# Kernel tuning notes

Hardware: AMD Instinct MI355X
Metric: run time of the kernel (lower is better)

Reference implementation:

```python
import jax, jax.numpy as jnp
import numpy as np
import math

B, L, D = 4, 4096, 768          # batch, seq_len (== l_max), d_model
ORDER, EMB_DIM = 16, 3          # hyena_filter_order, hyena_emb_dim
W_MOD = 1.0                     # hyena_w_mod
FAST, SLOW, TARGET = 0.3, 1.5, 1e-2  # ExponentialModulation defaults


def setup_inputs() -> dict:
    key = jax.random.key(0)
    ks = jax.random.split(key, 16)
    n = lambda i, shape, s: jax.random.normal(ks[i], shape, dtype=jnp.float32) * s
    # PositionalEmbedding buffer/param z, deterministic Hyena init (seq_len = l_max = L)
    t = np.linspace(0.0, 1.0, L)[None, :, None]
    bands = (EMB_DIM - 1) // 2
    t_re = np.linspace(0, L - 1, L)[None, :, None]
    w = 2 * math.pi * t_re / L
    f = np.linspace(1e-4, bands - 1, bands)[None, None]
    zc = np.exp(-1j * f * w)
    z = np.concatenate([t, zc.real, zc.imag], axis=-1).astype(np.float32)  # (1, L, 3)
    return {
        "u": jax.random.normal(ks[0], (B, L, D), dtype=jnp.float32),
        "w_in": n(1, (3 * D, D), 0.02),
        "b_in": jnp.zeros((3 * D,), jnp.float32),
        "w_out": n(2, (D, D), 0.02),
        "b_out": jnp.zeros((D,), jnp.float32),
        "conv_w": n(3, (3 * D, 1, 3), 0.3),   # depthwise Conv1d weight (O, I/groups=1, K)
        "conv_b": jnp.zeros((3 * D,), jnp.float32),
        "z": jnp.asarray(z),
        "fw1": n(4, (ORDER, EMB_DIM), 0.3),
        "fb1": n(5, (ORDER,), 0.3),
        "fw2": n(6, (ORDER, ORDER), 0.3),
        "fb2": n(7, (ORDER,), 0.3),
        "fw3": n(8, (ORDER, ORDER), 0.3),
        "fb3": n(9, (ORDER,), 0.3),
        "fw4": n(10, (D, ORDER), 0.3),
        "freq": jnp.full((1, ORDER), 10.0, jnp.float32),  # shared Sin freq, init w*ones
        "filter_bias": jax.random.normal(ks[11], (D,), dtype=jnp.float32),
    }


def _hyena_filter(z, fw1, fb1, fw2, fb2, fw3, fb3, fw4, freq, Lq):
    # implicit MLP with SHARED Sin activation (same freq param at all 3 activations)
    sin = lambda h: jnp.sin(W_MOD * freq * h)
    h = sin(z @ fw1.T + fb1)
    h = sin(h @ fw2.T + fb2)
    h = sin(h @ fw3.T + fb3)
    h = h @ fw4.T                                     # (1, L, D)
    # ExponentialModulation
    max_d = math.log(TARGET) / FAST
    min_d = math.log(TARGET) / SLOW
    deltas = jnp.linspace(min_d, max_d, D)[None, None]  # (1, 1, D)
    t = jnp.linspace(0.0, 1.0, Lq)[None, :, None]       # (1, L, 1)
    h = h * jnp.exp(-t * jnp.abs(deltas))
    return h[0].T                                      # (D, L)


def _fftconv(v, k, bias):
    # causal FFT long conv: fft_size = 2L, torch norm='forward' conventions
    Lq = v.shape[-1]
    nfft = 2 * Lq
    k_f = jnp.fft.rfft(k, n=nfft) / nfft               # (D, nfft//2+1)
    v_f = jnp.fft.rfft(v, n=nfft)                      # (B, D, nfft//2+1)
    y = jnp.fft.irfft(v_f * k_f, n=nfft, norm="forward")[..., :Lq]
    return y + v * bias[None, :, None]


def reference(u, w_in, b_in, w_out, b_out, conv_w, conv_b, z,
              fw1, fb1, fw2, fb2, fw3, fb3, fw4, freq, filter_bias):
    Bq, Lq, Dq = u.shape
    x = u @ w_in.T + b_in                              # (B, L, 3D)
    x = x.transpose(0, 2, 1)                           # (B, 3D, L)
    # depthwise short conv, kernel 3, padding 2, sliced to [:L]
    xc = jax.lax.conv_general_dilated(
        x, conv_w, window_strides=(1,), padding=[(2, 2)],
        feature_group_count=3 * Dq,
        dimension_numbers=("NCH", "OIH", "NCH"))[..., :Lq]
    xc = xc + conv_b[None, :, None]
    x1, x2, v = jnp.split(xc, 3, axis=1)               # each (B, D, L)
    v = v * x1                                         # pre-gate
    k = _hyena_filter(z[:, :Lq], fw1, fb1, fw2, fb2, fw3, fb3, fw4, freq, Lq)
    y = _fftconv(v, k, filter_bias) * x2               # long conv + post-gate
    y = y.transpose(0, 2, 1) @ w_out.T + b_out         # (B, L, D)
    return y
```

## Files before the change

### kernel.cpp

```cpp
#include <hip/hip_runtime.h>

#define BB 4
#define LL 4096
#define DD 768
#define TD 2304
#define NFFT 8192
#define PI2 6.283185307179586f

__device__ __forceinline__ unsigned short f2b(float f) {
    unsigned u = __float_as_uint(f);
    unsigned r = (u + 0x7fffu + ((u >> 16) & 1u)) >> 16;
    return (unsigned short)r;
}

typedef __bf16 bf16x8 __attribute__((ext_vector_type(8)));
typedef float  f32x4  __attribute__((ext_vector_type(4)));

constexpr float TWC[16] = {
    1.f, 0.98078528f, 0.92387953f, 0.83146961f,
    0.70710678f, 0.55557023f, 0.38268343f, 0.19509032f,
    0.f, -0.19509032f, -0.38268343f, -0.55557023f,
    -0.70710678f, -0.83146961f, -0.92387953f, -0.98078528f};
constexpr float TWS[16] = {
    0.f, 0.19509032f, 0.38268343f, 0.55557023f,
    0.70710678f, 0.83146961f, 0.92387953f, 0.98078528f,
    1.f, 0.98078528f, 0.92387953f, 0.83146961f,
    0.70710678f, 0.55557023f, 0.38268343f, 0.19509032f};

template<int LOGN, bool INV>
__device__ __forceinline__ void reg_fft(float2* R) {
    constexpr int N = 1 << LOGN;
#pragma unroll
    for (int i = 0; i < N; ++i) {
        int j = 0;
#pragma unroll
        for (int b = 0; b < LOGN; ++b) if (i & (1 << b)) j |= (1 << (LOGN - 1 - b));
        if (j > i) { float2 tt = R[i]; R[i] = R[j]; R[j] = tt; }
    }
#pragma unroll
    for (int s = 1; s <= LOGN; ++s) {
        const int hm = 1 << (s - 1);
        const int tsh = 5 - s;
#pragma unroll
        for (int g = 0; g < N; g += (hm << 1)) {
#pragma unroll
            for (int j2 = 0; j2 < hm; ++j2) {
                const float wr = TWC[j2 << tsh];
                const float wi = INV ? TWS[j2 << tsh] : -TWS[j2 << tsh];
                float2 u = R[g + j2];
                float2 v = R[g + j2 + hm];
                float vr = v.x * wr - v.y * wi;
                float vi = v.x * wi + v.y * wr;
                R[g + j2]      = make_float2(u.x + vr, u.y + vi);
                R[g + j2 + hm] = make_float2(u.x - vr, u.y - vi);
            }
        }
    }
}

template<int NN>
__device__ __forceinline__ void ramp_mul(float2* R, float ang) {
    float s0, c0; __sincosf(ang, &s0, &c0);
    float wr = c0, wi = s0;
#pragma unroll
    for (int k = 1; k < NN; ++k) {
        float xr = R[k].x, xi = R[k].y;
        R[k] = make_float2(xr * wr - xi * wi, xr * wi + xi * wr);
        float nr = wr * c0 - wi * s0;
        float ni = wr * s0 + wi * c0;
        wr = nr; wi = ni;
    }
}

#define A1(t, k2) ((k2) * 288 + (t) + ((t) >> 3))
#define A2(k2, p, r) ((k2) * 272 + (r) * 17 + (p))
#define FFT_LDS 9216

__device__ __forceinline__ void eng_fwd(float2* buf, float2* R, int t) {
    reg_fft<5, false>(R);
    ramp_mul<32>(R, -PI2 * (float)t / 8192.0f);
    __syncthreads();
#pragma unroll
    for (int k2 = 0; k2 < 32; ++k2) buf[A1(t, k2)] = R[k2];
    __syncthreads();
    const int p = t & 15, c2 = (t >> 4) << 1;
#pragma unroll
    for (int q = 0; q < 16; ++q) {
        R[q]      = buf[A1(p + 16 * q, c2)];
        R[16 + q] = buf[A1(p + 16 * q, c2 + 1)];
    }
    reg_fft<4, false>(R);
    reg_fft<4, false>(R + 16);
    float a2 = -PI2 * (float)p / 256.0f;
    ramp_mul<16>(R, a2);
    ramp_mul<16>(R + 16, a2);
    __syncthreads();
#pragma unroll
    for (int r = 0; r < 16; ++r) {
        buf[A2(c2, p, r)]     = R[r];
        buf[A2(c2 + 1, p, r)] = R[16 + r];
    }
    __syncthreads();
    const int rr = p;
#pragma unroll
    for (int pp = 0; pp < 16; ++pp) {
        R[pp]      = buf[A2(c2, pp, rr)];
        R[16 + pp] = buf[A2(c2 + 1, pp, rr)];
    }
    reg_fft<4, false>(R);
    reg_fft<4, false>(R + 16);
}

__device__ __forceinline__ void eng_inv(float2* buf, float2* R, int t) {
    const int p = t & 15, c2 = (t >> 4) << 1, rr = p;
    reg_fft<4, true>(R);
    reg_fft<4, true>(R + 16);
    __syncthreads();
#pragma unroll
    for (int pp = 0; pp < 16; ++pp) {
        buf[A2(c2, pp, rr)]     = R[pp];
        buf[A2(c2 + 1, pp, rr)] = R[16 + pp];
    }
    __syncthreads();
#pragma unroll
    for (int r = 0; r < 16; ++r) {
        R[r]      = buf[A2(c2, p, r)];
        R[16 + r] = buf[A2(c2 + 1, p, r)];
    }
    float a2 = PI2 * (float)p / 256.0f;
    ramp_mul<16>(R, a2);
    ramp_mul<16>(R + 16, a2);
    reg_fft<4, true>(R);
    reg_fft<4, true>(R + 16);
    __syncthreads();
#pragma unroll
    for (int q = 0; q < 16; ++q) {
        buf[A1(p + 16 * q, c2)]     = R[q];
        buf[A1(p + 16 * q, c2 + 1)] = R[16 + q];
    }
    __syncthreads();
#pragma unroll
    for (int k2 = 0; k2 < 32; ++k2) R[k2] = buf[A1(t, k2)];
    ramp_mul<32>(R, PI2 * (float)t / 8192.0f);
    reg_fft<5, true>(R);
}

__global__ __launch_bounds__(256) void k_cast_pair(
        const float* __restrict__ srcA, unsigned long long nA4,
        const float* __restrict__ srcB, unsigned long long nB4,
        unsigned short* __restrict__ dstA, unsigned short* __restrict__ dstB) {
    unsigned long long i = (unsigned long long)blockIdx.x * 256 + threadIdx.x;
    const float* s; unsigned short* d;
    if (i < nA4)            { s = srcA + i * 4;         d = dstA + i * 4; }
    else if (i < nA4 + nB4) { unsigned long long j = i - nA4; s = srcB + j * 4; d = dstB + j * 4; }
    else return;
    float4 v = *(const float4*)s;
    unsigned long long p = (unsigned long long)f2b(v.x)
                         | ((unsigned long long)f2b(v.y) << 16)
                         | ((unsigned long long)f2b(v.z) << 32)
                         | ((unsigned long long)f2b(v.w) << 48);
    *(unsigned long long*)d = p;
}

__global__ __launch_bounds__(256) void k_gemm_mfma(
        const unsigned short* __restrict__ A, const unsigned short* __restrict__ Bw,
        const float* __restrict__ bias, float* __restrict__ C,
        int N, int K) {
    __shared__ unsigned char AsB[8192];
    __shared__ unsigned char BsB[8192];
    const int tid  = threadIdx.x;
    const int lane = tid & 63;
    const int w    = tid >> 6;
    const int wr   = w >> 1, wc = w & 1;
    const int m0 = blockIdx.y * 128, n0 = blockIdx.x * 128;
    f32x4 acc[4][4] = {};
    const int rowIn = lane >> 2;
    const int k16   = lane & 3;
    for (int k0 = 0; k0 < K; k0 += 32) {
#pragma unroll
        for (int c = 0; c < 2; ++c) {
            int chunk = w * 2 + c;
            int row = chunk * 16 + rowIn;
            const char* ga = (const char*)A  + (((size_t)(m0 + row) * K + k0) * 2) + k16 * 16;
            __builtin_amdgcn_global_load_lds(
                (const __attribute__((address_space(1))) void*)ga,
                (__attribute__((address_space(3))) void*)(AsB + chunk * 1024), 16, 0, 0);
            const char* gb = (const char*)Bw + (((size_t)(n0 + row) * K + k0) * 2) + k16 * 16;
            __builtin_amdgcn_global_load_lds(
                (const __attribute__((address_space(1))) void*)gb,
                (__attribute__((address_space(3))) void*)(BsB + chunk * 1024), 16, 0, 0);
        }
        __syncthreads();
        const int koff = (lane >> 4) * 16;
        const int rsel = lane & 15;
        bf16x8 af[4], bfr[4];
#pragma unroll
        for (int i = 0; i < 4; ++i) {
            af[i]  = *(const bf16x8*)(AsB + (wr * 64 + i * 16 + rsel) * 64 + koff);
            bfr[i] = *(const bf16x8*)(BsB + (wc * 64 + i * 16 + rsel) * 64 + koff);
        }
#pragma unroll
        for (int i = 0; i < 4; ++i)
#pragma unroll
            for (int j = 0; j < 4; ++j)
                acc[i][j] = __builtin_amdgcn_mfma_f32_16x16x32_bf16(af[i], bfr[j], acc[i][j], 0, 0, 0);
        __syncthreads();
    }
    const int cq = lane >> 4;
    const int cn = lane & 15;
#pragma unroll
    for (int j = 0; j < 4; ++j) {
        int col = n0 + wc * 64 + j * 16 + cn;
        float bv = bias[col];
#pragma unroll
        for (int i = 0; i < 4; ++i) {
            int rbase = m0 + wr * 64 + i * 16 + cq * 4;
#pragma unroll
            for (int r = 0; r < 4; ++r)
                C[(size_t)(rbase + r) * N + col] = acc[i][j][r] + bv;
        }
    }
}

__global__ __launch_bounds__(256) void k_shortconv(
        const float* __restrict__ x, const float* __restrict__ conv_w,
        const float* __restrict__ conv_b,
        float* __restrict__ vbuf, float* __restrict__ x2buf) {
    __shared__ float xs[3][32][66];
    const int l0 = blockIdx.x * 64;
    const int d0 = blockIdx.y * 32;
    const int b  = blockIdx.z;
    const int tid = threadIdx.x;
    for (int idx = tid; idx < 3 * 66 * 32; idx += 256) {
        int g  = idx / (66 * 32);
        int r  = idx % (66 * 32);
        int ll = r >> 5;
        int dd = r & 31;
        int gl = l0 - 2 + ll;
        float val = 0.f;
        if (gl >= 0) val = x[((size_t)(b * LL + gl)) * TD + g * DD + d0 + dd];
        xs[g][dd][ll] = val;
    }
    __syncthreads();
    const int tl  = tid & 63;
    const int tdq = tid >> 6;
    for (int dd = tdq; dd < 32; dd += 4) {
        int c0 = d0 + dd;
        const float* w0 = conv_w + (size_t)c0 * 3;
        const float* w1 = conv_w + (size_t)(DD + c0) * 3;
        const float* w2 = conv_w + (size_t)(2 * DD + c0) * 3;
        float x1v = w0[0]*xs[0][dd][tl] + w0[1]*xs[0][dd][tl+1] + w0[2]*xs[0][dd][tl+2] + conv_b[c0];
        float x2v = w1[0]*xs[1][dd][tl] + w1[1]*xs[1][dd][tl+1] + w1[2]*xs[1][dd][tl+2] + conv_b[DD + c0];
        float vv  = w2[0]*xs[2][dd][tl] + w2[1]*xs[2][dd][tl+1] + w2[2]*xs[2][dd][tl+2] + conv_b[2*DD + c0];
        size_t o = ((size_t)(b * DD + c0)) * LL + l0 + tl;
        vbuf[o]  = vv * x1v;
        x2buf[o] = x2v;
    }
}

__global__ __launch_bounds__(256) void k_filter_mlp(
        const float* __restrict__ z,
        const float* __restrict__ fw1, const float* __restrict__ fb1,
        const float* __restrict__ fw2, const float* __restrict__ fb2,
        const float* __restrict__ fw3, const float* __restrict__ fb3,
        const float* __restrict__ freq, float* __restrict__ h3g) {
    int l = blockIdx.x * 256 + threadIdx.x;
    float z0 = z[l*3+0], z1 = z[l*3+1], z2 = z[l*3+2];
    float h1[16], h2[16];
#pragma unroll
    for (int j = 0; j < 16; ++j) {
        float a = z0*fw1[j*3+0] + z1*fw1[j*3+1] + z2*fw1[j*3+2] + fb1[j];
        h1[j] = sinf(freq[j] * a);
    }
#pragma unroll
    for (int j = 0; j < 16; ++j) {
        float a = fb2[j];
#pragma unroll
        for (int i = 0; i < 16; ++i) a += h1[i] * fw2[j*16+i];
        h2[j] = sinf(freq[j] * a);
    }
#pragma unroll
    for (int j = 0; j < 16; ++j) {
        float a = fb3[j];
#pragma unroll
        for (int i = 0; i < 16; ++i) a += h2[i] * fw3[j*16+i];
        h3g[j * LL + l] = sinf(freq[j] * a);
    }
}

__global__ __launch_bounds__(256) void k_filter_fft(
        const float* __restrict__ h3g, const float* __restrict__ fw4,
        const float* __restrict__ fbias, float2* __restrict__ kf) {
    __shared__ float2 buf[FFT_LDS];
    const int d = blockIdx.x, t = threadIdx.x;
    float w4[16];
#pragma unroll
    for (int i = 0; i < 16; ++i) w4[i] = fw4[d * 16 + i];
    const float min_d = 3.070113457325394f;
    const float max_d = 15.35056728662697f;
    const float ad = min_d + (max_d - min_d) * ((float)d / 767.0f);
    float2 R[32];
#pragma unroll
    for (int j = 0; j < 16; ++j) {
        int l = t + 256 * j;
        float acc = 0.f;
#pragma unroll
        for (int i = 0; i < 16; ++i) acc += h3g[i * LL + l] * w4[i];
        acc *= __expf(-((float)l / 4095.0f) * ad);
        R[j] = make_float2(acc, 0.f);
        R[16 + j] = make_float2(0.f, 0.f);
    }
    eng_fwd(buf, R, t);
    const float fb = fbias[d];
    const float inv_n = 1.0f / (float)NFFT;
    float2* kd = kf + (size_t)d * NFFT;
#pragma unroll
    for (int i = 0; i < 32; ++i)
        kd[i * 256 + t] = make_float2((R[i].x + fb) * inv_n, R[i].y * inv_n);
}

__global__ __launch_bounds__(256) void k_fftconv3(
        const float* __restrict__ vbuf, const float2* __restrict__ kf,
        float* __restrict__ x2y) {
    __shared__ float2 buf[FFT_LDS];
    const int bp = blockIdx.x;
    const int d = bp % DD;
    const int bpair = bp / DD;
    const size_t row1 = (size_t)(bpair * 2) * DD + d;
    const size_t row2 = row1 + DD;
    const float* v1 = vbuf + row1 * LL;
    const float* v2 = vbuf + row2 * LL;
    const int t = threadIdx.x;
    float2 R[32];
#pragma unroll
    for (int j = 0; j < 16; ++j) {
        int idx = t + 256 * j;
        R[j] = make_float2(v1[idx], v2[idx]);
        R[16 + j] = make_float2(0.f, 0.f);
    }
    eng_fwd(buf, R, t);
    const float2* kd = kf + (size_t)d * NFFT;
#pragma unroll
    for (int i = 0; i < 32; ++i) {
        float2 w = kd[i * 256 + t];
        float2 zv = R[i];
        R[i] = make_float2(zv.x * w.x - zv.y * w.y, zv.x * w.y + zv.y * w.x);
    }
    eng_inv(buf, R, t);
    float* o1 = x2y + row1 * LL;
    float* o2 = x2y + row2 * LL;
#pragma unroll
    for (int j = 0; j < 16; ++j) {
        int idx = t + 256 * j;
        o1[idx] = R[j].x * o1[idx];
        o2[idx] = R[j].y * o2[idx];
    }
}

__global__ __launch_bounds__(256) void k_transpose_cast(
        const float* __restrict__ yg, unsigned short* __restrict__ ygT) {
    __shared__ float t[64][65];
    const int b = blockIdx.z;
    const int d0 = blockIdx.y * 64;
    const int l0 = blockIdx.x * 64;
    for (int idx = threadIdx.x; idx < 4096; idx += 256) {
        int r = idx >> 6, c = idx & 63;
        t[r][c] = yg[((size_t)(b * DD + d0 + r)) * LL + l0 + c];
    }
    __syncthreads();
    for (int idx = threadIdx.x; idx < 2048; idx += 256) {
        int r = idx >> 5, c = (idx & 31) * 2;
        unsigned int p = (unsigned int)f2b(t[c][r]) | ((unsigned int)f2b(t[c+1][r]) << 16);
        *(unsigned int*)&ygT[((size_t)(b * LL + l0 + r)) * DD + d0 + c] = p;
    }
}

extern "C" void kernel_launch(void* const* d_in, const int* in_sizes, int n_in,
                              void* d_out, int out_size, void* d_ws, size_t ws_size,
                              hipStream_t stream) {
    const float* u      = (const float*)d_in[0];
    const float* w_in   = (const float*)d_in[1];
    const float* b_in   = (const float*)d_in[2];
    const float* w_out  = (const float*)d_in[3];
    const float* b_out  = (const float*)d_in[4];
    const float* conv_w = (const float*)d_in[5];
    const float* conv_b = (const float*)d_in[6];
    const float* z      = (const float*)d_in[7];
    const float* fw1    = (const float*)d_in[8];
    const float* fb1    = (const float*)d_in[9];
    const float* fw2    = (const float*)d_in[10];
    const float* fb2    = (const float*)d_in[11];
    const float* fw3    = (const float*)d_in[12];
    const float* fb3    = (const float*)d_in[13];
    const float* fw4    = (const float*)d_in[14];
    const float* freq   = (const float*)d_in[15];
    const float* fbias  = (const float*)d_in[16];

    char* ws = (char*)d_ws;
    float*  x        = (float*)(ws);
    float2* kf       = (float2*)(ws);
    float*  h3g      = (float*)(ws + 50331648);
    unsigned short* w_out_bf = (unsigned short*)(ws + 50593792);
    unsigned short* ygT      = (unsigned short*)(ws + 63176704);
    float*  vbuf     = (float*)(ws + 150994944);
    float*  x2y      = (float*)(ws + 201326592);
    unsigned short* u_bf     = (unsigned short*)(ws + 201326592);
    unsigned short* w_in_bf  = (unsigned short*)(ws + 226492416);

    k_cast_pair<<<(3145728 + 442368 + 255) / 256, 256, 0, stream>>>(
        u, 3145728ULL, w_in, 442368ULL, u_bf, w_in_bf);
    k_gemm_mfma<<<dim3(TD/128, (BB*LL)/128), 256, 0, stream>>>(u_bf, w_in_bf, b_in, x, TD, DD);
    k_shortconv<<<dim3(LL/64, DD/32, BB), 256, 0, stream>>>(x, conv_w, conv_b, vbuf, x2y);
    k_filter_mlp<<<LL/256, 256, 0, stream>>>(z, fw1, fb1, fw2, fb2, fw3, fb3, freq, h3g);
    k_filter_fft<<<DD, 256, 0, stream>>>(h3g, fw4, fbias, kf);
    k_cast_pair<<<(147456 + 255) / 256, 256, 0, stream>>>(
        w_out, 147456ULL, (const float*)0, 0ULL, w_out_bf, (unsigned short*)0);
    k_fftconv3<<<(BB/2)*DD, 256, 0, stream>>>(vbuf, kf, x2y);
    k_transpose_cast<<<dim3(LL/64, DD/64, BB), 256, 0, stream>>>(x2y, ygT);
    k_gemm_mfma<<<dim3(DD/128, (BB*LL)/128), 256, 0, stream>>>(ygT, w_out_bf, b_out, (float*)d_out, DD, DD);
}
```

Measured before the change: 449.4 us.

## Store intermediates in bf16 and widen GEMM K-tile with XOR-swizzled LDS

The input projection GEMM now writes bf16 instead of fp32, and the short-conv, FFT-conv and transpose kernels read and write their intermediate buffers (x, v, x2/y) in bf16. This halves the HBM traffic of the memory-bound stages between the two GEMMs. The GEMM also moves to a 64-wide K tile with an XOR-swizzled shared-memory layout, which cuts the number of barriers per tile and is meant to avoid LDS bank conflicts. In exchange, intermediate activations lose precision, which increases numerical error.

```diff
diff --git a/kernel.cpp b/kernel.cpp
--- a/kernel.cpp
+++ b/kernel.cpp
@@ -11,6 +11,9 @@
     unsigned u = __float_as_uint(f);
     unsigned r = (u + 0x7fffu + ((u >> 16) & 1u)) >> 16;
     return (unsigned short)r;
+}
+__device__ __forceinline__ float b2f(unsigned short h) {
+    return __uint_as_float((unsigned)h << 16);
 }
 
 typedef __bf16 bf16x8 __attribute__((ext_vector_type(8)));
@@ -162,84 +165,105 @@
     *(unsigned long long*)d = p;
 }
 
+#define GEMM_BODY(EPILOGUE)                                                     \
+    __shared__ unsigned char AsB[16384];                                        \
+    __shared__ unsigned char BsB[16384];                                        \
+    const int tid  = threadIdx.x;                                               \
+    const int lane = tid & 63;                                                  \
+    const int w    = tid >> 6;                                                  \
+    const int wr   = w >> 1, wc = w & 1;                                        \
+    const int m0 = blockIdx.y * 128, n0 = blockIdx.x * 128;                     \
+    f32x4 acc[4][4] = {};                                                       \
+    const int srow = lane >> 3;                    \
+    const int sslot = (lane & 7) ^ srow;          \
+    for (int k0 = 0; k0 < K; k0 += 64) {                                        \
+        _Pragma("unroll")                                                       \
+        for (int c = 0; c < 4; ++c) {                                           \
+            int chunk = w * 4 + c;                                              \
+            int row = chunk * 8 + srow;                                         \
+            const char* ga = (const char*)A  + (((size_t)(m0 + row) * K + k0) * 2) + sslot * 16; \
+            __builtin_amdgcn_global_load_lds(                                   \
+                (const __attribute__((address_space(1))) void*)ga,              \
+                (__attribute__((address_space(3))) void*)(AsB + chunk * 1024), 16, 0, 0); \
+            const char* gb = (const char*)Bw + (((size_t)(n0 + row) * K + k0) * 2) + sslot * 16; \
+            __builtin_amdgcn_global_load_lds(                                   \
+                (const __attribute__((address_space(1))) void*)gb,              \
+                (__attribute__((address_space(3))) void*)(BsB + chunk * 1024), 16, 0, 0); \
+        }                                                                       \
+        __syncthreads();                                                        \
+        const int quad = lane >> 4;                                             \
+        const int rsel = lane & 15;                                             \
+        _Pragma("unroll")                                                       \
+        for (int kk = 0; kk < 2; ++kk) {                                        \
+            bf16x8 af[4], bfr[4];                                               \
+            _Pragma("unroll")                                                   \
+            for (int i = 0; i < 4; ++i) {                                       \
+                int rowA = wr * 64 + i * 16 + rsel;                             \
+                int slotA = (kk * 4 + quad) ^ (rsel & 7);                       \
+                af[i]  = *(const bf16x8*)(AsB + rowA * 128 + slotA * 16);       \
+                int rowB = wc * 64 + i * 16 + rsel;                             \
+                bfr[i] = *(const bf16x8*)(BsB + rowB * 128 + slotA * 16);       \
+            }                                                                   \
+            _Pragma("unroll")                                                   \
+            for (int i = 0; i < 4; ++i)                                         \
+                _Pragma("unroll")                                               \
+                for (int j = 0; j < 4; ++j)                                     \
+                    acc[i][j] = __builtin_amdgcn_mfma_f32_16x16x32_bf16(af[i], bfr[j], acc[i][j], 0, 0, 0); \
+        }                                                                       \
+        __syncthreads();                                                        \
+    }                                                                           \
+    const int cq = lane >> 4;                                                   \
+    const int cn = lane & 15;                                                   \
+    _Pragma("unroll")                                                           \
+    for (int j = 0; j < 4; ++j) {                                               \
+        int col = n0 + wc * 64 + j * 16 + cn;                                   \
+        float bv = bias[col];                                                   \
+        _Pragma("unroll")                                                       \
+        for (int i = 0; i < 4; ++i) {                                           \
+            int rbase = m0 + wr * 64 + i * 16 + cq * 4;                         \
+            _Pragma("unroll")                                                   \
+            for (int r = 0; r < 4; ++r)                                         \
+                EPILOGUE;                                                       \
+        }                                                                       \
+    }
+
+__global__ __launch_bounds__(256) void k_gemm_mfma_b16(
+        const unsigned short* __restrict__ A, const unsigned short* __restrict__ Bw,
+        const float* __restrict__ bias, unsigned short* __restrict__ C,
+        int N, int K) {
+    GEMM_BODY(C[(size_t)(rbase + r) * N + col] = f2b(acc[i][j][r] + bv))
+}
+
 __global__ __launch_bounds__(256) void k_gemm_mfma(
         const unsigned short* __restrict__ A, const unsigned short* __restrict__ Bw,
         const float* __restrict__ bias, float* __restrict__ C,
         int N, int K) {
-    __shared__ unsigned char AsB[8192];
-    __shared__ unsigned char BsB[8192];
-    const int tid  = threadIdx.x;
-    const int lane = tid & 63;
-    const int w    = tid >> 6;
-    const int wr   = w >> 1, wc = w & 1;
-    const int m0 = blockIdx.y * 128, n0 = blockIdx.x * 128;
-    f32x4 acc[4][4] = {};
-    const int rowIn = lane >> 2;
-    const int k16   = lane & 3;
-    for (int k0 = 0; k0 < K; k0 += 32) {
-#pragma unroll
-        for (int c = 0; c < 2; ++c) {
-            int chunk = w * 2 + c;
-            int row = chunk * 16 + rowIn;
-            const char* ga = (const char*)A  + (((size_t)(m0 + row) * K + k0) * 2) + k16 * 16;
-            __builtin_amdgcn_global_load_lds(
-                (const __attribute__((address_space(1))) void*)ga,
-                (__attribute__((address_space(3))) void*)(AsB + chunk * 1024), 16, 0, 0);
-            const char* gb = (const char*)Bw + (((size_t)(n0 + row) * K + k0) * 2) + k16 * 16;
-            __builtin_amdgcn_global_load_lds(
-                (const __attribute__((address_space(1))) void*)gb,
-                (__attribute__((address_space(3))) void*)(BsB + chunk * 1024), 16, 0, 0);
-        }
-        __syncthreads();
-        const int koff = (lane >> 4) * 16;
-        const int rsel = lane & 15;
-        bf16x8 af[4], bfr[4];
-#pragma unroll
-        for (int i = 0; i < 4; ++i) {
-            af[i]  = *(const bf16x8*)(AsB + (wr * 64 + i * 16 + rsel) * 64 + koff);
-            bfr[i] = *(const bf16x8*)(BsB + (wc * 64 + i * 16 + rsel) * 64 + koff);
-        }
-#pragma unroll
-        for (int i = 0; i < 4; ++i)
-#pragma unroll
-            for (int j = 0; j < 4; ++j)
-                acc[i][j] = __builtin_amdgcn_mfma_f32_16x16x32_bf16(af[i], bfr[j], acc[i][j], 0, 0, 0);
-        __syncthreads();
-    }
-    const int cq = lane >> 4;
-    const int cn = lane & 15;
-#pragma unroll
-    for (int j = 0; j < 4; ++j) {
-        int col = n0 + wc * 64 + j * 16 + cn;
-        float bv = bias[col];
-#pragma unroll
-        for (int i = 0; i < 4; ++i) {
-            int rbase = m0 + wr * 64 + i * 16 + cq * 4;
-#pragma unroll
-            for (int r = 0; r < 4; ++r)
-                C[(size_t)(rbase + r) * N + col] = acc[i][j][r] + bv;
-        }
-    }
+    GEMM_BODY(C[(size_t)(rbase + r) * N + col] = acc[i][j][r] + bv)
 }
 
 __global__ __launch_bounds__(256) void k_shortconv(
-        const float* __restrict__ x, const float* __restrict__ conv_w,
+        const unsigned short* __restrict__ x, const float* __restrict__ conv_w,
         const float* __restrict__ conv_b,
-        float* __restrict__ vbuf, float* __restrict__ x2buf) {
+        unsigned short* __restrict__ vbuf, unsigned short* __restrict__ x2buf) {
     __shared__ float xs[3][32][66];
     const int l0 = blockIdx.x * 64;
     const int d0 = blockIdx.y * 32;
     const int b  = blockIdx.z;
     const int tid = threadIdx.x;
-    for (int idx = tid; idx < 3 * 66 * 32; idx += 256) {
-        int g  = idx / (66 * 32);
-        int r  = idx % (66 * 32);
-        int ll = r >> 5;
-        int dd = r & 31;
+    for (int idx = tid; idx < 3 * 66 * 16; idx += 256) {
+        int g  = idx / (66 * 16);
+        int r  = idx % (66 * 16);
+        int ll = r >> 4;
+        int dd2 = (r & 15) * 2;
         int gl = l0 - 2 + ll;
-        float val = 0.f;
-        if (gl >= 0) val = x[((size_t)(b * LL + gl)) * TD + g * DD + d0 + dd];
-        xs[g][dd][ll] = val;
+        float v0 = 0.f, v1 = 0.f;
+        if (gl >= 0) {
+            unsigned int pk = *(const unsigned int*)&x[((size_t)(b * LL + gl)) * TD + g * DD + d0 + dd2];
+            v0 = b2f((unsigned short)(pk & 0xffffu));
+            v1 = b2f((unsigned short)(pk >> 16));
+        }
+        xs[g][dd2][ll] = v0;
+        xs[g][dd2 + 1][ll] = v1;
     }
     __syncthreads();
     const int tl  = tid & 63;
@@ -253,8 +277,8 @@
         float x2v = w1[0]*xs[1][dd][tl] + w1[1]*xs[1][dd][tl+1] + w1[2]*xs[1][dd][tl+2] + conv_b[DD + c0];
         float vv  = w2[0]*xs[2][dd][tl] + w2[1]*xs[2][dd][tl+1] + w2[2]*xs[2][dd][tl+2] + conv_b[2*DD + c0];
         size_t o = ((size_t)(b * DD + c0)) * LL + l0 + tl;
-        vbuf[o]  = vv * x1v;
-        x2buf[o] = x2v;
+        vbuf[o]  = f2b(vv * x1v);
+        x2buf[o] = f2b(x2v);
     }
 }
 
@@ -320,22 +344,22 @@
 }
 
 __global__ __launch_bounds__(256) void k_fftconv3(
-        const float* __restrict__ vbuf, const float2* __restrict__ kf,
-        float* __restrict__ x2y) {
+        const unsigned short* __restrict__ vbuf, const float2* __restrict__ kf,
+        unsigned short* __restrict__ x2y) {
     __shared__ float2 buf[FFT_LDS];
     const int bp = blockIdx.x;
     const int d = bp % DD;
     const int bpair = bp / DD;
     const size_t row1 = (size_t)(bpair * 2) * DD + d;
     const size_t row2 = row1 + DD;
-    const float* v1 = vbuf + row1 * LL;
-    const float* v2 = vbuf + row2 * LL;
+    const unsigned short* v1 = vbuf + row1 * LL;
+    const unsigned short* v2 = vbuf + row2 * LL;
     const int t = threadIdx.x;
     float2 R[32];
 #pragma unroll
     for (int j = 0; j < 16; ++j) {
         int idx = t + 256 * j;
-        R[j] = make_float2(v1[idx], v2[idx]);
+        R[j] = make_float2(b2f(v1[idx]), b2f(v2[idx]));
         R[16 + j] = make_float2(0.f, 0.f);
     }
     eng_fwd(buf, R, t);
@@ -347,25 +371,25 @@
         R[i] = make_float2(zv.x * w.x - zv.y * w.y, zv.x * w.y + zv.y * w.x);
     }
     eng_inv(buf, R, t);
-    float* o1 = x2y + row1 * LL;
-    float* o2 = x2y + row2 * LL;
+    unsigned short* o1 = x2y + row1 * LL;
+    unsigned short* o2 = x2y + row2 * LL;
 #pragma unroll
     for (int j = 0; j < 16; ++j) {
         int idx = t + 256 * j;
-        o1[idx] = R[j].x * o1[idx];
-        o2[idx] = R[j].y * o2[idx];
+        o1[idx] = f2b(R[j].x * b2f(o1[idx]));
+        o2[idx] = f2b(R[j].y * b2f(o2[idx]));
     }
 }
 
 __global__ __launch_bounds__(256) void k_transpose_cast(
-        const float* __restrict__ yg, unsigned short* __restrict__ ygT) {
+        const unsigned short* __restrict__ yg, unsigned short* __restrict__ ygT) {
     __shared__ float t[64][65];
     const int b = blockIdx.z;
     const int d0 = blockIdx.y * 64;
     const int l0 = blockIdx.x * 64;
     for (int idx = threadIdx.x; idx < 4096; idx += 256) {
         int r = idx >> 6, c = idx & 63;
-        t[r][c] = yg[((size_t)(b * DD + d0 + r)) * LL + l0 + c];
+        t[r][c] = b2f(yg[((size_t)(b * DD + d0 + r)) * LL + l0 + c]);
     }
     __syncthreads();
     for (int idx = threadIdx.x; idx < 2048; idx += 256) {
@@ -397,20 +421,20 @@
     const float* fbias  = (const float*)d_in[16];
 
     char* ws = (char*)d_ws;
-    float*  x        = (float*)(ws);
-    float2* kf       = (float2*)(ws);
-    float*  h3g      = (float*)(ws + 50331648);
+    unsigned short* x_bf     = (unsigned short*)(ws);
+    float2* kf               = (float2*)(ws);
+    float*  h3g              = (float*)(ws + 50331648);
     unsigned short* w_out_bf = (unsigned short*)(ws + 50593792);
     unsigned short* ygT      = (unsigned short*)(ws + 63176704);
-    float*  vbuf     = (float*)(ws + 150994944);
-    float*  x2y      = (float*)(ws + 201326592);
+    unsigned short* vbuf     = (unsigned short*)(ws + 150994944);
+    unsigned short* x2y      = (unsigned short*)(ws + 176160768);
     unsigned short* u_bf     = (unsigned short*)(ws + 201326592);
     unsigned short* w_in_bf  = (unsigned short*)(ws + 226492416);
 
     k_cast_pair<<<(3145728 + 442368 + 255) / 256, 256, 0, stream>>>(
         u, 3145728ULL, w_in, 442368ULL, u_bf, w_in_bf);
-    k_gemm_mfma<<<dim3(TD/128, (BB*LL)/128), 256, 0, stream>>>(u_bf, w_in_bf, b_in, x, TD, DD);
-    k_shortconv<<<dim3(LL/64, DD/32, BB), 256, 0, stream>>>(x, conv_w, conv_b, vbuf, x2y);
+    k_gemm_mfma_b16<<<dim3(TD/128, (BB*LL)/128), 256, 0, stream>>>(u_bf, w_in_bf, b_in, x_bf, TD, DD);
+    k_shortconv<<<dim3(LL/64, DD/32, BB), 256, 0, stream>>>(x_bf, conv_w, conv_b, vbuf, x2y);
     k_filter_mlp<<<LL/256, 256, 0, stream>>>(z, fw1, fb1, fw2, fb2, fw3, fb3, freq, h3g);
     k_filter_fft<<<DD, 256, 0, stream>>>(h3g, fw4, fbias, kf);
     k_cast_pair<<<(147456 + 255) / 256, 256, 0, stream>>>(
```

Result: faster. 427.2 us (-4.9%).
